# Kernel tuning notes

Measured on AMD Instinct MI355X. Metric: run time of the kernel, lower is better.

The kernel has to match this reference:

```python
import jax, jax.numpy as jnp
import numpy as np

N_USERS = 16384
EMB_DIM = 32
N_EDGES = 524288  # N_USERS * avg_degree 32


def setup_inputs() -> dict:
    key = jax.random.key(0)
    k1, k2, k3, k4, k5 = jax.random.split(key, 5)
    social_emb = jax.random.normal(k1, (N_USERS, EMB_DIM), dtype=jnp.float32)
    preference_emb = jax.random.normal(k2, (N_USERS, EMB_DIM), dtype=jnp.float32)
    # Jaccard similarities lie in [0, 1]
    attention_scores = jax.random.uniform(k3, (N_USERS, N_USERS), dtype=jnp.float32)
    uu_graph = jax.random.randint(k4, (2, N_EDGES), 0, N_USERS, dtype=jnp.int64)
    return {
        "social_emb": social_emb,
        "preference_emb": preference_emb,
        "attention_scores": attention_scores,
        "uu_graph": uu_graph,
    }


def reference(social_emb, preference_emb, attention_scores, uu_graph):
    # The original per-user Python loop:
    #   final[i] = sum_j attention_scores[i, j] * preference_emb[j]
    # is exactly one dense [N,N] @ [N,D] matmul.
    final = attention_scores @ preference_emb  # [N, D]
    # prop_uu: one round of message passing over the user-user graph
    # (sum of source-user embeddings into each destination user).
    src, dst = uu_graph[0], uu_graph[1]
    out = jax.ops.segment_sum(final[src], dst, num_segments=final.shape[0])  # [N, D]
    # dropout is identity at inference (rate treated as 0)
    return out
```

## Files before the change

### kernel.cpp

```cpp
#include <hip/hip_runtime.h>
#include <hip/hip_bf16.h>

#define NUSERS 16384
#define DIM 32
#define NEDGES 524288
#define KCHUNK 32
#define KTILE 256
#define NTILES (NUSERS / KTILE)
#define RPB 64
#define CAP 192

using f32x4  = __attribute__((ext_vector_type(4))) float;
using bf16x8 = __attribute__((ext_vector_type(8))) short;
using s16x4  = __attribute__((ext_vector_type(4))) short;
using int4v  = __attribute__((ext_vector_type(4))) int;
using int2v  = __attribute__((ext_vector_type(2))) int;

static __device__ __forceinline__ short f2bf(float f) {
    __hip_bfloat16 h = __float2bfloat16(f);
    return __builtin_bit_cast(short, h);
}

static __device__ __forceinline__ bool detect_is64(const int* __restrict__ g) {
    bool is64 = true;
#pragma unroll
    for (int s = 0; s < 8; ++s) is64 &= (g[2 * s + 1] == 0);
    return is64;
}

__global__ void __launch_bounds__(256) prep_and_bucket(const float* __restrict__ P,
                                                       short* __restrict__ Pfrag,
                                                       const int* __restrict__ g,
                                                       int* __restrict__ cursor,
                                                       int* __restrict__ bucket) {
    if (blockIdx.x < 256) {
        int t = blockIdx.x * blockDim.x + threadIdx.x;
        int lane = t & 63;
        int h    = (t >> 6) & 1;
        int c    = t >> 7;
        int d    = h * 16 + (lane & 15);
        int gq   = lane >> 4;
        short tmp[8];
#pragma unroll
        for (int i = 0; i < 8; ++i)
            tmp[i] = f2bf(P[(size_t)(c * KCHUNK + gq * 8 + i) * DIM + d]);
        *reinterpret_cast<bf16x8*>(Pfrag + (size_t)t * 8) =
            *reinterpret_cast<bf16x8*>(tmp);
    } else {
        bool is64 = detect_is64(g);
        int e = (blockIdx.x - 256) * blockDim.x + threadIdx.x;
        int src, dst;
        if (is64) {
            const int2v* g2 = reinterpret_cast<const int2v*>(g);
            src = g2[e].x;
            dst = g2[NEDGES + e].x;
        } else {
            src = g[e];
            dst = g[NEDGES + e];
        }
        int p = atomicAdd(&cursor[dst], 1);
        if (p < CAP) bucket[(size_t)dst * CAP + p] = src;
    }
}

__global__ void __launch_bounds__(256, 1) gemm_kernel(const float* __restrict__ A,
                                                      const short* __restrict__ Pfrag,
                                                      float* __restrict__ fin) {
    __shared__ short lds[4][2][16][256];

    const int lane = threadIdx.x & 63;
    const int wave = threadIdx.x >> 6;
    const int r    = lane & 15;
    const int gq   = lane >> 4;

    const int row0 = blockIdx.x * RPB + wave * 16;
    const float* Abase = A + (size_t)row0 * NUSERS;

    short* buf0 = &lds[wave][0][0][0];
    short* buf1 = &lds[wave][1][0][0];

    f32x4  acc0 = {0.f, 0.f, 0.f, 0.f};
    f32x4  acc1 = {0.f, 0.f, 0.f, 0.f};
    f32x4  sreg[16];
    bf16x8 bregA[16], bregB[16];

    auto issueA = [&](int t) {
#pragma unroll
        for (int k = 0; k < 16; ++k)
            sreg[k] = *reinterpret_cast<const f32x4*>(
                Abase + (size_t)k * NUSERS + t * KTILE + lane * 4);
    };
    auto issueB = [&](int t, bf16x8* br) {
        const short* pf = Pfrag + (size_t)t * 8192;
#pragma unroll
        for (int cc = 0; cc < 8; ++cc) {
            br[2 * cc]     = *reinterpret_cast<const bf16x8*>(pf + cc * 1024 + lane * 8);
            br[2 * cc + 1] = *reinterpret_cast<const bf16x8*>(pf + cc * 1024 + 512 + lane * 8);
        }
    };
    auto commitT = [&](short* buf) {
#pragma unroll
        for (int k = 0; k < 16; ++k) {
            int cb = (lane * 8) ^ ((k & 7) << 4);
            s16x4 v = {f2bf(sreg[k][0]), f2bf(sreg[k][1]),
                       f2bf(sreg[k][2]), f2bf(sreg[k][3])};
            *reinterpret_cast<s16x4*>(buf + k * 256 + (cb >> 1)) = v;
        }
        asm volatile("s_waitcnt lgkmcnt(0)" ::: "memory");
        __builtin_amdgcn_sched_barrier(0);
    };
    auto computeT = [&](const bf16x8* br, const short* buf) {
#pragma unroll
        for (int cc = 0; cc < 8; ++cc) {
            int cb = (cc * 64 + gq * 16) ^ ((r & 7) << 4);
            bf16x8 af = *reinterpret_cast<const bf16x8*>(buf + r * 256 + (cb >> 1));
            acc0 = __builtin_amdgcn_mfma_f32_16x16x32_bf16(af, br[2 * cc],     acc0, 0, 0, 0);
            acc1 = __builtin_amdgcn_mfma_f32_16x16x32_bf16(af, br[2 * cc + 1], acc1, 0, 0, 0);
        }
    };

    issueB(0, bregA);
    issueA(0);
    commitT(buf0);

    for (int t = 0; t < NTILES; t += 2) {
        issueB(t + 1, bregB);
        issueA(t + 1);
        computeT(bregA, buf0);
        commitT(buf1);
        if (t + 2 < NTILES) {
            issueB(t + 2, bregA);
            issueA(t + 2);
        }
        computeT(bregB, buf1);
        if (t + 2 < NTILES) commitT(buf0);
    }

    const int out_row0 = row0 + gq * 4;
#pragma unroll
    for (int q = 0; q < 4; ++q) {
        float* dst = fin + (size_t)(out_row0 + q) * DIM + r;
        dst[0]  = acc0[q];
        dst[16] = acc1[q];
    }
}

__global__ void __launch_bounds__(256) gather_kernel(const int* __restrict__ bucket,
                                                     const int* __restrict__ cursor,
                                                     const float* __restrict__ fin,
                                                     float* __restrict__ out) {
    int t = blockIdx.x * blockDim.x + threadIdx.x;
    int d = t >> 3;
    int q = t & 7;
    if (d >= NUSERS) return;
    int cnt = cursor[d];
    if (cnt > CAP) cnt = CAP;
    const int* bk = bucket + (size_t)d * CAP;
    const f32x4* f4 = reinterpret_cast<const f32x4*>(fin);
    f32x4 s = {0.f, 0.f, 0.f, 0.f};
    int i = 0;
    for (; i + 4 <= cnt; i += 4) {
        int4v s4 = *reinterpret_cast<const int4v*>(bk + i);
        s += f4[(size_t)s4.x * 8 + q];
        s += f4[(size_t)s4.y * 8 + q];
        s += f4[(size_t)s4.z * 8 + q];
        s += f4[(size_t)s4.w * 8 + q];
    }
    for (; i < cnt; ++i)
        s += f4[(size_t)bk[i] * 8 + q];
    reinterpret_cast<f32x4*>(out)[(size_t)d * 8 + q] = s;
}

extern "C" void kernel_launch(void* const* d_in, const int* in_sizes, int n_in,
                              void* d_out, int out_size, void* d_ws, size_t ws_size,
                              hipStream_t stream) {
    const float* pref = (const float*)d_in[1];
    const float* att  = (const float*)d_in[2];
    const int*   grph = (const int*)d_in[3];
    float* out = (float*)d_out;

    char* ws = (char*)d_ws;
    float* fin    = (float*)ws;
    short* pfrag  = (short*)(ws + (size_t)18 * 1024 * 1024);
    int*   cursor = (int*)  (ws + (size_t)19 * 1024 * 1024);
    int*   bucket = (int*)  (ws + (size_t)20 * 1024 * 1024);

    hipMemsetAsync(cursor, 0, NUSERS * sizeof(int), stream);

    prep_and_bucket<<<dim3(256 + NEDGES / 256), dim3(256), 0, stream>>>(
        pref, pfrag, grph, cursor, bucket);

    gemm_kernel<<<dim3(NUSERS / RPB), dim3(256), 0, stream>>>(att, pfrag, fin);

    gather_kernel<<<dim3(NUSERS * 8 / 256), dim3(256), 0, stream>>>(bucket, cursor, fin, out);
}
```

Measured before the change: 218.7 us.

## Halve GEMM K-tile to raise occupancy and split gather edges across lane pairs

The GEMM K-tile shrinks from 256 to 128. Per-wave A loads now cover two rows at 128 columns each, and launch bounds rise to allow two blocks per CU, which cuts register and LDS use so more waves can hide HBM latency on the dense attention read. The gather kernel now uses two threads per output float4, each taking alternate edges into four independent accumulators before a shuffle reduction, to add memory-level parallelism. In exchange, the shorter tiles mean more loop iterations and more barrier overhead per byte loaded.

```diff
diff --git a/kernel.cpp b/kernel.cpp
--- a/kernel.cpp
+++ b/kernel.cpp
@@ -5,7 +5,7 @@
 #define DIM 32
 #define NEDGES 524288
 #define KCHUNK 32
-#define KTILE 256
+#define KTILE 128
 #define NTILES (NUSERS / KTILE)
 #define RPB 64
 #define CAP 192
@@ -13,7 +13,6 @@
 using f32x4  = __attribute__((ext_vector_type(4))) float;
 using bf16x8 = __attribute__((ext_vector_type(8))) short;
 using s16x4  = __attribute__((ext_vector_type(4))) short;
-using int4v  = __attribute__((ext_vector_type(4))) int;
 using int2v  = __attribute__((ext_vector_type(2))) int;
 
 static __device__ __forceinline__ short f2bf(float f) {
@@ -63,10 +62,10 @@
     }
 }
 
-__global__ void __launch_bounds__(256, 1) gemm_kernel(const float* __restrict__ A,
+__global__ void __launch_bounds__(256, 2) gemm_kernel(const float* __restrict__ A,
                                                       const short* __restrict__ Pfrag,
                                                       float* __restrict__ fin) {
-    __shared__ short lds[4][2][16][256];
+    __shared__ short lds[4][2][16][128];
 
     const int lane = threadIdx.x & 63;
     const int wave = threadIdx.x >> 6;
@@ -76,44 +75,48 @@
     const int row0 = blockIdx.x * RPB + wave * 16;
     const float* Abase = A + (size_t)row0 * NUSERS;
 
+    const int srow  = lane >> 5;
+    const int scolf = (lane & 31) * 4;
+
     short* buf0 = &lds[wave][0][0][0];
     short* buf1 = &lds[wave][1][0][0];
 
     f32x4  acc0 = {0.f, 0.f, 0.f, 0.f};
     f32x4  acc1 = {0.f, 0.f, 0.f, 0.f};
-    f32x4  sreg[16];
-    bf16x8 bregA[16], bregB[16];
+    f32x4  sreg[8];
+    bf16x8 bregA[8], bregB[8];
 
     auto issueA = [&](int t) {
 #pragma unroll
-        for (int k = 0; k < 16; ++k)
+        for (int k = 0; k < 8; ++k)
             sreg[k] = *reinterpret_cast<const f32x4*>(
-                Abase + (size_t)k * NUSERS + t * KTILE + lane * 4);
+                Abase + (size_t)(2 * k + srow) * NUSERS + t * KTILE + scolf);
     };
     auto issueB = [&](int t, bf16x8* br) {
-        const short* pf = Pfrag + (size_t)t * 8192;
-#pragma unroll
-        for (int cc = 0; cc < 8; ++cc) {
+        const short* pf = Pfrag + (size_t)t * 4096;
+#pragma unroll
+        for (int cc = 0; cc < 4; ++cc) {
             br[2 * cc]     = *reinterpret_cast<const bf16x8*>(pf + cc * 1024 + lane * 8);
             br[2 * cc + 1] = *reinterpret_cast<const bf16x8*>(pf + cc * 1024 + 512 + lane * 8);
         }
     };
     auto commitT = [&](short* buf) {
 #pragma unroll
-        for (int k = 0; k < 16; ++k) {
-            int cb = (lane * 8) ^ ((k & 7) << 4);
+        for (int k = 0; k < 8; ++k) {
+            int rl = 2 * k + srow;
+            int cb = ((lane & 31) * 8) ^ ((rl & 7) << 4);
             s16x4 v = {f2bf(sreg[k][0]), f2bf(sreg[k][1]),
                        f2bf(sreg[k][2]), f2bf(sreg[k][3])};
-            *reinterpret_cast<s16x4*>(buf + k * 256 + (cb >> 1)) = v;
+            *reinterpret_cast<s16x4*>(buf + rl * 128 + (cb >> 1)) = v;
         }
         asm volatile("s_waitcnt lgkmcnt(0)" ::: "memory");
         __builtin_amdgcn_sched_barrier(0);
     };
     auto computeT = [&](const bf16x8* br, const short* buf) {
 #pragma unroll
-        for (int cc = 0; cc < 8; ++cc) {
+        for (int cc = 0; cc < 4; ++cc) {
             int cb = (cc * 64 + gq * 16) ^ ((r & 7) << 4);
-            bf16x8 af = *reinterpret_cast<const bf16x8*>(buf + r * 256 + (cb >> 1));
+            bf16x8 af = *reinterpret_cast<const bf16x8*>(buf + r * 128 + (cb >> 1));
             acc0 = __builtin_amdgcn_mfma_f32_16x16x32_bf16(af, br[2 * cc],     acc0, 0, 0, 0);
             acc1 = __builtin_amdgcn_mfma_f32_16x16x32_bf16(af, br[2 * cc + 1], acc1, 0, 0, 0);
         }
@@ -150,25 +153,34 @@
                                                      const float* __restrict__ fin,
                                                      float* __restrict__ out) {
     int t = blockIdx.x * blockDim.x + threadIdx.x;
-    int d = t >> 3;
-    int q = t & 7;
+    int d = t >> 4;
+    int q = (t >> 1) & 7;
+    int h = t & 1;
     if (d >= NUSERS) return;
     int cnt = cursor[d];
     if (cnt > CAP) cnt = CAP;
     const int* bk = bucket + (size_t)d * CAP;
     const f32x4* f4 = reinterpret_cast<const f32x4*>(fin);
-    f32x4 s = {0.f, 0.f, 0.f, 0.f};
-    int i = 0;
-    for (; i + 4 <= cnt; i += 4) {
-        int4v s4 = *reinterpret_cast<const int4v*>(bk + i);
-        s += f4[(size_t)s4.x * 8 + q];
-        s += f4[(size_t)s4.y * 8 + q];
-        s += f4[(size_t)s4.z * 8 + q];
-        s += f4[(size_t)s4.w * 8 + q];
-    }
-    for (; i < cnt; ++i)
-        s += f4[(size_t)bk[i] * 8 + q];
-    reinterpret_cast<f32x4*>(out)[(size_t)d * 8 + q] = s;
+    f32x4 s0 = {0.f, 0.f, 0.f, 0.f};
+    f32x4 s1 = {0.f, 0.f, 0.f, 0.f};
+    f32x4 s2 = {0.f, 0.f, 0.f, 0.f};
+    f32x4 s3 = {0.f, 0.f, 0.f, 0.f};
+    int i = h;
+    for (; i + 6 < cnt; i += 8) {
+        s0 += f4[(size_t)bk[i]     * 8 + q];
+        s1 += f4[(size_t)bk[i + 2] * 8 + q];
+        s2 += f4[(size_t)bk[i + 4] * 8 + q];
+        s3 += f4[(size_t)bk[i + 6] * 8 + q];
+    }
+    for (; i < cnt; i += 2)
+        s0 += f4[(size_t)bk[i] * 8 + q];
+    f32x4 s = (s0 + s1) + (s2 + s3);
+    s.x += __shfl_xor(s.x, 1);
+    s.y += __shfl_xor(s.y, 1);
+    s.z += __shfl_xor(s.z, 1);
+    s.w += __shfl_xor(s.w, 1);
+    if (h == 0)
+        reinterpret_cast<f32x4*>(out)[(size_t)d * 8 + q] = s;
 }
 
 extern "C" void kernel_launch(void* const* d_in, const int* in_sizes, int n_in,
@@ -192,5 +204,5 @@
 
     gemm_kernel<<<dim3(NUSERS / RPB), dim3(256), 0, stream>>>(att, pfrag, fin);
 
-    gather_kernel<<<dim3(NUSERS * 8 / 256), dim3(256), 0, stream>>>(bucket, cursor, fin, out);
-}
+    gather_kernel<<<dim3(NUSERS * 16 / 256), dim3(256), 0, stream>>>(bucket, cursor, fin, out);
+}
```

After: 234.8 us. +7.4%, slower.
